# Kernel optimization log

Measured on AMD Instinct MI355X. Metric: run time of the kernel, lower is better.

Reference implementation:

```python
import jax, jax.numpy as jnp
import numpy as np
import math

D, H, F = 1024, 16, 4096
DH = D // H
EPS_LN = 1e-5


def _layernorm(x, scale, bias):
    mu = jnp.mean(x, axis=-1, keepdims=True)
    var = jnp.mean(jnp.square(x - mu), axis=-1, keepdims=True)
    return (x - mu) * jax.lax.rsqrt(var + EPS_LN) * scale + bias


def setup_inputs() -> dict:
    key = jax.random.key(0)
    ks = jax.random.split(key, 16)
    B, T = 2, 2048
    src = jax.random.normal(ks[0], (B, T, D), dtype=jnp.float32)
    attn_mask = jax.random.randint(ks[1], (T, T), 0, 2) == 1  # bool [T,S], True = masked
    xavier = lambda k, shp: jax.random.uniform(k, shp, jnp.float32, -1.0, 1.0) * math.sqrt(6.0 / (shp[0] + shp[1]))
    return {
        "src": src, "attn_mask": attn_mask,
        "q_w": xavier(ks[2], (D, D)), "q_b": jnp.zeros((D,), jnp.float32),
        "k_w": xavier(ks[3], (D, D)), "k_b": jnp.zeros((D,), jnp.float32),
        "v_w": xavier(ks[4], (D, D)), "v_b": jnp.zeros((D,), jnp.float32),
        "o_w": xavier(ks[5], (D, D)), "o_b": jnp.zeros((D,), jnp.float32),
        "l1_w": xavier(ks[6], (F, D)), "l1_b": jnp.zeros((F,), jnp.float32),
        "l2_w": xavier(ks[7], (D, F)), "l2_b": jnp.zeros((D,), jnp.float32),
        "n1_s": jnp.ones((D,), jnp.float32), "n1_b": jnp.zeros((D,), jnp.float32),
        "n2_s": jnp.ones((D,), jnp.float32), "n2_b": jnp.zeros((D,), jnp.float32),
        "alpha_attn": jax.random.normal(ks[8], (), jnp.float32) * 0.1,
        "alpha_ff": jax.random.normal(ks[9], (), jnp.float32) * 0.1,
    }


def reference(src, attn_mask, q_w, q_b, k_w, k_b, v_w, v_b, o_w, o_b,
              l1_w, l1_b, l2_w, l2_b, n1_s, n1_b, n2_s, n2_b,
              alpha_attn, alpha_ff):
    B, T, _ = src.shape
    # --- self-attention block (post-norm layer, dropout=0 => identity) ---
    q = (src @ q_w.T + q_b).reshape(B, T, H, DH).transpose(0, 2, 1, 3)  # [B,H,T,DH]
    k = (src @ k_w.T + k_b).reshape(B, T, H, DH).transpose(0, 2, 1, 3)
    v = (src @ v_w.T + v_b).reshape(B, T, H, DH).transpose(0, 2, 1, 3)
    scores = jnp.einsum('bhtd,bhsd->bhts', q, k) / math.sqrt(DH)  # [B,H,T,S]
    scores = jnp.where(attn_mask[None, None, :, :], -jnp.inf, scores)
    probs = jax.nn.softmax(scores + 1e-9, axis=-1)
    probs = jnp.where(jnp.isinf(scores), 0.0, probs)  # zero where masked (custom semantics)
    attn = jnp.einsum('bhts,bhsd->bhtd', probs, v).transpose(0, 2, 1, 3).reshape(B, T, D)
    attn = attn @ o_w.T + o_b
    x = _layernorm(src + alpha_attn * attn, n1_s, n1_b)
    # --- FFN block ---
    ff = jax.nn.relu(x @ l1_w.T + l1_b) @ l2_w.T + l2_b
    x = _layernorm(x + alpha_ff * ff, n2_s, n2_b)
    return x
```

## Files before the change

### kernel.cpp

```cpp
#include <hip/hip_runtime.h>
#include <math.h>

#define Dm 1024
#define Hh 16
#define DHd 64
#define Ff 4096
#define Tt 2048
#define Bb 2

#define ATT_C2 0.18033688011112042f

typedef __bf16 bf16_8 __attribute__((ext_vector_type(8)));
typedef __bf16 bf16x2 __attribute__((ext_vector_type(2)));
typedef __bf16 bf16x4 __attribute__((ext_vector_type(4)));
typedef float  f32x4  __attribute__((ext_vector_type(4)));

__device__ __forceinline__ unsigned short f2bf(float f) {
    unsigned int u = __float_as_uint(f);
    unsigned int r = (u + 0x7fffu + ((u >> 16) & 1u)) >> 16;
    return (unsigned short)r;
}

__device__ __forceinline__ bf16x2 pkbf(float a, float b) {
#if __has_builtin(__builtin_amdgcn_cvt_pk_bf16_f32)
    return __builtin_amdgcn_cvt_pk_bf16_f32(a, b);
#else
    bf16x2 r; r[0] = (__bf16)a; r[1] = (__bf16)b; return r;
#endif
}
__device__ __forceinline__ bf16x4 pkbf4(float a, float b, float c, float d) {
    bf16x2 lo = pkbf(a, b), hi = pkbf(c, d);
    return __builtin_shufflevector(lo, hi, 0, 1, 2, 3);
}

__device__ __forceinline__ void gld_lds16(const void* g, void* l) {
    __builtin_amdgcn_global_load_lds(
        (const __attribute__((address_space(1))) void*)g,
        (__attribute__((address_space(3))) void*)l,
        16, 0, 0);
}

__global__ __launch_bounds__(256) void preprocess_kernel(
    const float* __restrict__ q_w, const float* __restrict__ k_w,
    const float* __restrict__ v_w, const float* __restrict__ o_w,
    const float* __restrict__ l1_w, const float* __restrict__ l2_w,
    const float* __restrict__ src, const int* __restrict__ mask,
    const float* __restrict__ q_b, const float* __restrict__ k_b,
    unsigned short* __restrict__ qkw, unsigned short* __restrict__ vw16,
    unsigned short* __restrict__ ow,  unsigned short* __restrict__ l1w,
    unsigned short* __restrict__ l2w, unsigned short* __restrict__ srcb,
    unsigned* __restrict__ mbit, float* __restrict__ qkb)
{
    const int bid = blockIdx.x;
    const int tid = threadIdx.x;
    if (bid < 16384) {
        int i = bid * 256 + tid;
        const float* sp; unsigned short* dp; int off;
        if (i < 1048576) {
            if (i < 262144)      { sp = q_w; dp = qkw;           off = i; }
            else if (i < 524288) { sp = k_w; dp = qkw + 1048576; off = i - 262144; }
            else if (i < 786432) { sp = v_w; dp = vw16;          off = i - 524288; }
            else                 { sp = o_w; dp = ow;            off = i - 786432; }
        } else if (i < 2097152)  { sp = l1_w; dp = l1w;          off = i - 1048576; }
        else if (i < 3145728)    { sp = l2_w; dp = l2w;          off = i - 2097152; }
        else                     { sp = src;  dp = srcb;         off = i - 3145728; }
        float4 v = ((const float4*)sp)[off];
        ((bf16x4*)dp)[off] = pkbf4(v.x, v.y, v.z, v.w);
    } else if (bid < 16896) {
        int w = (bid - 16384) * 256 + tid;
        const int* p = mask + (size_t)w * 32;
        unsigned bits = 0;
        #pragma unroll
        for (int j = 0; j < 8; ++j) {
            int4 v = ((const int4*)p)[j];
            bits |= (v.x != 0 ? 1u : 0u) << (j * 4 + 0);
            bits |= (v.y != 0 ? 1u : 0u) << (j * 4 + 1);
            bits |= (v.z != 0 ? 1u : 0u) << (j * 4 + 2);
            bits |= (v.w != 0 ? 1u : 0u) << (j * 4 + 3);
        }
        mbit[w] = bits;
    } else {
        int i = (bid - 16896) * 256 + tid;
        qkb[i] = (i < 1024) ? q_b[i] : k_b[i - 1024];
    }
}

template<int RELU, int BF16OUT>
__global__ __launch_bounds__(256) void gemm_bf16_kernel(
    const unsigned short* __restrict__ A, const unsigned short* __restrict__ W,
    const float* __restrict__ bias, void* __restrict__ C, void* __restrict__ C2,
    int M, int N, int K, int ldc, int ksub)
{
    __shared__ __bf16 As[128][64];
    __shared__ __bf16 Bs[128][64];
    const int tid  = threadIdx.x;
    const int lane = tid & 63;
    const int wave = tid >> 6;
    const int m0 = blockIdx.y * 128;
    const int n0 = blockIdx.x * 128;
    const int lr8 = lane >> 3;
    const int gch = (lane & 7) ^ lr8;
    const int wm = (wave & 1) * 64;
    const int wn = (wave >> 1) * 64;
    const int quad = lane >> 4;
    const int lm = lane & 15;
    const int z  = blockIdx.z;
    const int kstart = z * ksub;
    void* Cz = (z == 0) ? C : C2;

    f32x4 acc[4][4];
    #pragma unroll
    for (int i = 0; i < 4; i++)
        #pragma unroll
        for (int j = 0; j < 4; j++) {
            acc[i][j][0] = 0.f; acc[i][j][1] = 0.f;
            acc[i][j][2] = 0.f; acc[i][j][3] = 0.f;
        }

    for (int k0 = kstart; k0 < kstart + ksub; k0 += 64) {
        __syncthreads();
        #pragma unroll
        for (int i = 0; i < 4; i++) {
            int seg = wave * 4 + i;
            int r = seg * 8 + lr8;
            gld_lds16(A + (size_t)(m0 + r) * K + k0 + gch * 8, &As[seg * 8][0]);
            gld_lds16(W + (size_t)(n0 + r) * K + k0 + gch * 8, &Bs[seg * 8][0]);
        }
        __syncthreads();
        #pragma unroll
        for (int kh = 0; kh < 2; kh++) {
            bf16_8 af[4], bfr[4];
            #pragma unroll
            for (int t = 0; t < 4; t++) {
                int ch = (kh * 4 + quad) ^ (lm & 7);
                af[t]  = *(const bf16_8*)&As[wm + t * 16 + lm][ch * 8];
                bfr[t] = *(const bf16_8*)&Bs[wn + t * 16 + lm][ch * 8];
            }
            #pragma unroll
            for (int i = 0; i < 4; i++)
                #pragma unroll
                for (int j = 0; j < 4; j++)
                    acc[i][j] = __builtin_amdgcn_mfma_f32_16x16x32_bf16(
                        af[i], bfr[j], acc[i][j], 0, 0, 0);
        }
    }

    float bvc[4];
    #pragma unroll
    for (int j = 0; j < 4; j++)
        bvc[j] = (z == 0) ? bias[n0 + wn + j * 16 + lm] : 0.f;

    #pragma unroll
    for (int i = 0; i < 4; i++)
        #pragma unroll
        for (int j = 0; j < 4; j++) {
            int col = n0 + wn + j * 16 + lm;
            #pragma unroll
            for (int r = 0; r < 4; r++) {
                int row = m0 + wm + i * 16 + quad * 4 + r;
                float v = acc[i][j][r] + bvc[j];
                if (RELU) v = fmaxf(v, 0.f);
                if (BF16OUT)
                    ((unsigned short*)Cz)[(size_t)row * ldc + col] = f2bf(v);
                else
                    ((float*)Cz)[(size_t)row * ldc + col] = v;
            }
        }
}

__global__ __launch_bounds__(256) void gemm_qkvt_kernel(
    const unsigned short* __restrict__ srcb, const unsigned short* __restrict__ qkw,
    const unsigned short* __restrict__ vw16, const float* __restrict__ qkb,
    const float* __restrict__ v_b,
    unsigned short* __restrict__ qk16, unsigned short* __restrict__ vtf)
{
    const int bid = blockIdx.x;
    const unsigned short *A, *W;
    const float* bias;
    unsigned short* C;
    int m0, n0, ldc;
    bool qscale, rowbias;
    if (bid < 512) {
        A = srcb; W = qkw; bias = qkb; C = qk16;
        n0 = (bid & 15) * 128; m0 = (bid >> 4) * 128;
        ldc = 2048; qscale = true; rowbias = false;
    } else {
        int b2 = bid - 512;
        A = vw16; W = srcb; bias = v_b; C = vtf;
        n0 = (b2 & 31) * 128; m0 = (b2 >> 5) * 128;
        ldc = 4096; qscale = false; rowbias = true;
    }
    const int K = 1024;

    __shared__ __bf16 As[128][64];
    __shared__ __bf16 Bs[128][64];
    const int tid  = threadIdx.x;
    const int lane = tid & 63;
    const int wave = tid >> 6;
    const int lr8 = lane >> 3;
    const int gch = (lane & 7) ^ lr8;
    const int wm = (wave & 1) * 64;
    const int wn = (wave >> 1) * 64;
    const int quad = lane >> 4;
    const int lm = lane & 15;

    f32x4 acc[4][4];
    #pragma unroll
    for (int i = 0; i < 4; i++)
        #pragma unroll
        for (int j = 0; j < 4; j++) {
            acc[i][j][0] = 0.f; acc[i][j][1] = 0.f;
            acc[i][j][2] = 0.f; acc[i][j][3] = 0.f;
        }

    for (int k0 = 0; k0 < K; k0 += 64) {
        __syncthreads();
        #pragma unroll
        for (int i = 0; i < 4; i++) {
            int seg = wave * 4 + i;
            int r = seg * 8 + lr8;
            gld_lds16(A + (size_t)(m0 + r) * K + k0 + gch * 8, &As[seg * 8][0]);
            gld_lds16(W + (size_t)(n0 + r) * K + k0 + gch * 8, &Bs[seg * 8][0]);
        }
        __syncthreads();
        #pragma unroll
        for (int kh = 0; kh < 2; kh++) {
            bf16_8 af[4], bfr[4];
            #pragma unroll
            for (int t = 0; t < 4; t++) {
                int ch = (kh * 4 + quad) ^ (lm & 7);
                af[t]  = *(const bf16_8*)&As[wm + t * 16 + lm][ch * 8];
                bfr[t] = *(const bf16_8*)&Bs[wn + t * 16 + lm][ch * 8];
            }
            #pragma unroll
            for (int i = 0; i < 4; i++)
                #pragma unroll
                for (int j = 0; j < 4; j++)
                    acc[i][j] = __builtin_amdgcn_mfma_f32_16x16x32_bf16(
                        af[i], bfr[j], acc[i][j], 0, 0, 0);
        }
    }

    float bvc[4];
    float brr[4][4];
    if (!rowbias) {
        #pragma unroll
        for (int j = 0; j < 4; j++) bvc[j] = bias[n0 + wn + j * 16 + lm];
    } else {
        #pragma unroll
        for (int i = 0; i < 4; i++) {
            float4 t4 = *(const float4*)&bias[m0 + wm + i * 16 + quad * 4];
            brr[i][0] = t4.x; brr[i][1] = t4.y; brr[i][2] = t4.z; brr[i][3] = t4.w;
        }
    }

    #pragma unroll
    for (int i = 0; i < 4; i++)
        #pragma unroll
        for (int j = 0; j < 4; j++) {
            int col = n0 + wn + j * 16 + lm;
            #pragma unroll
            for (int r = 0; r < 4; r++) {
                int row = m0 + wm + i * 16 + quad * 4 + r;
                float v = acc[i][j][r] + (rowbias ? brr[i][r] : bvc[j]);
                if (qscale && col < 1024) v *= ATT_C2;
                C[(size_t)row * ldc + col] = f2bf(v);
            }
        }
}

__global__ __launch_bounds__(256) void attn_mfma_kernel(
    const unsigned short* __restrict__ qk,
    const unsigned short* __restrict__ vt,
    const unsigned* __restrict__ mb,
    float* __restrict__ opart,
    float* __restrict__ lpart)
{
    __shared__ __bf16 Ks[128 * 64];
    __shared__ __bf16 Vt[64 * 128];
    __shared__ __bf16 Ps[4][32 * 64];

    const int tid  = threadIdx.x;
    const int lane = tid & 63;
    const int wave = tid >> 6;
    const int c    = lane & 15;
    const int quad = lane >> 4;
    const int bh = blockIdx.y;
    const int b = bh >> 4, h = bh & 15;
    const int t0 = blockIdx.x * 128;
    const int tw = t0 + wave * 32;
    const int z  = blockIdx.z;

    bf16_8 qf[2][2];
    #pragma unroll
    for (int tt = 0; tt < 2; ++tt)
        #pragma unroll
        for (int ks = 0; ks < 2; ++ks)
            qf[tt][ks] = *(const bf16_8*)(qk +
                (size_t)(b * Tt + tw + tt * 16 + c) * 2048 +
                h * DHd + quad * 8 + ks * 32);

    f32x4 oacc[2][4];
    f32x4 ol[2];
    #pragma unroll
    for (int tt = 0; tt < 2; ++tt) {
        ol[tt][0] = 0.f; ol[tt][1] = 0.f; ol[tt][2] = 0.f; ol[tt][3] = 0.f;
        #pragma unroll
        for (int dt = 0; dt < 4; ++dt) {
            oacc[tt][dt][0] = 0.f; oacc[tt][dt][1] = 0.f;
            oacc[tt][dt][2] = 0.f; oacc[tt][dt][3] = 0.f;
        }
    }
    bf16_8 vone;
    {
        __bf16 one = (__bf16)1.0f;
        #pragma unroll
        for (int j = 0; j < 8; ++j) vone[j] = one;
    }

    const int krow8 = lane >> 3;
    const int kj    = (lane & 7) ^ krow8;
    const int vr4   = lane >> 4;

    for (int st16 = z * 8; st16 < z * 8 + 8; ++st16) {
        const int s0 = st16 * 128;
        __syncthreads();

        #pragma unroll
        for (int i = 0; i < 4; ++i) {
            int ci = wave * 4 + i;
            {
                int r = 8 * ci + krow8;
                const unsigned short* g = qk +
                    (size_t)(b * Tt + s0 + r) * 2048 + 1024 + h * DHd + kj * 8;
                gld_lds16(g, &Ks[ci * 512]);
            }
            {
                int d = 4 * ci + vr4;
                int jj = (lane & 15) ^ (d & 7);
                const unsigned short* g = vt +
                    (size_t)(h * DHd + d) * 4096 + b * Tt + s0 + jj * 8;
                gld_lds16(g, &Vt[ci * 512]);
            }
        }

        unsigned mwv[2][4];
        #pragma unroll
        for (int tt = 0; tt < 2; ++tt)
            #pragma unroll
            for (int sp = 0; sp < 4; ++sp)
                mwv[tt][sp] = mb[(size_t)(tw + tt * 16 + c) * 64 + (s0 >> 5) + sp];

        __syncthreads();

        #pragma unroll
        for (int half = 0; half < 2; ++half) {
            #pragma unroll
            for (int s8l = 0; s8l < 4; ++s8l) {
                const int s8 = half * 4 + s8l;
                bf16_8 kf0 = *(const bf16_8*)&Ks[((s8 * 16 + c) * 8 + ((quad + 0) ^ (c & 7))) * 8];
                bf16_8 kf1 = *(const bf16_8*)&Ks[((s8 * 16 + c) * 8 + ((quad + 4) ^ (c & 7))) * 8];
                #pragma unroll
                for (int tt = 0; tt < 2; ++tt) {
                    f32x4 zr; zr[0] = 0.f; zr[1] = 0.f; zr[2] = 0.f; zr[3] = 0.f;
                    zr = __builtin_amdgcn_mfma_f32_16x16x32_bf16(kf0, qf[tt][0], zr, 0, 0, 0);
                    f32x4 sv = __builtin_amdgcn_mfma_f32_16x16x32_bf16(kf1, qf[tt][1], zr, 0, 0, 0);
                    unsigned mword = mwv[tt][s8 >> 1];
                    int bp = (s8 & 1) * 16 + quad * 4;
                    float p[4];
                    #pragma unroll
                    for (int r = 0; r < 4; ++r) {
                        int bit = (mword >> (bp + r)) & 1;
                        float x = bit ? -1e30f : sv[r];
                        p[r] = __builtin_amdgcn_exp2f(x);
                    }
                    bf16x4 pk4v = pkbf4(p[0], p[1], p[2], p[3]);
                    int trow = tt * 16 + c;
                    int ch = (s8l * 2 + (quad >> 1)) ^ (c & 7);
                    *(bf16x4*)&Ps[wave][trow * 64 + ch * 8 + (quad & 1) * 4] = pk4v;
                }
            }
            #pragma unroll
            for (int ks = 0; ks < 2; ++ks) {
                bf16_8 pa[2], vf[4];
                #pragma unroll
                for (int tt = 0; tt < 2; ++tt) {
                    int ch = (ks * 4 + quad) ^ (c & 7);
                    pa[tt] = *(const bf16_8*)&Ps[wave][(tt * 16 + c) * 64 + ch * 8];
                }
                #pragma unroll
                for (int dt = 0; dt < 4; ++dt) {
                    int sc = half * 8 + ks * 4 + quad;
                    int d = dt * 16 + c;
                    vf[dt] = *(const bf16_8*)&Vt[(d * 16 + (sc ^ (c & 7))) * 8];
                }
                #pragma unroll
                for (int tt = 0; tt < 2; ++tt) {
                    #pragma unroll
                    for (int dt = 0; dt < 4; ++dt)
                        oacc[tt][dt] = __builtin_amdgcn_mfma_f32_16x16x32_bf16(
                            pa[tt], vf[dt], oacc[tt][dt], 0, 0, 0);
                    ol[tt] = __builtin_amdgcn_mfma_f32_16x16x32_bf16(
                        pa[tt], vone, ol[tt], 0, 0, 0);
                }
            }
        }
    }

    float* op = opart + (size_t)z * 4194304;
    #pragma unroll
    for (int tt = 0; tt < 2; ++tt)
        #pragma unroll
        for (int r = 0; r < 4; ++r) {
            int row = b * Tt + tw + tt * 16 + quad * 4 + r;
            #pragma unroll
            for (int dt = 0; dt < 4; ++dt)
                op[(size_t)row * Dm + h * DHd + dt * 16 + c] = oacc[tt][dt][r];
            if (c == 0)
                lpart[z * 65536 + row * 16 + h] = ol[tt][r];
        }
}

__global__ __launch_bounds__(256) void combine_kernel(
    const float* __restrict__ opart, const float* __restrict__ lpart,
    unsigned short* __restrict__ atb)
{
    const int row = blockIdx.x;
    const int tid = threadIdx.x;
    const int h = tid >> 4;
    float l = lpart[row * 16 + h] + lpart[65536 + row * 16 + h];
    float inv = (l > 0.f) ? 1.f / l : 0.f;
    float4 a = ((const float4*)(opart + (size_t)row * Dm))[tid];
    float4 b = ((const float4*)(opart + 4194304 + (size_t)row * Dm))[tid];
    ((bf16x4*)(atb + (size_t)row * Dm))[tid] =
        pkbf4((a.x + b.x) * inv, (a.y + b.y) * inv,
              (a.z + b.z) * inv, (a.w + b.w) * inv);
}

template<int NPARTS, int BASEBF, int OUTF32, int OUTBF>
__global__ __launch_bounds__(256) void residual_ln_kernel(
    const void* __restrict__ base, const float* __restrict__ d0,
    const float* __restrict__ d1,
    const float* __restrict__ alpha_p, const float* __restrict__ scale,
    const float* __restrict__ bias, float* __restrict__ out,
    unsigned short* __restrict__ out_bf)
{
    const int row = blockIdx.x;
    const int tid = threadIdx.x;
    const float alpha = alpha_p[0];
    float4 xb;
    if (BASEBF) {
        bf16x4 bb = ((const bf16x4*)((const unsigned short*)base + (size_t)row * Dm))[tid];
        xb.x = (float)bb[0]; xb.y = (float)bb[1]; xb.z = (float)bb[2]; xb.w = (float)bb[3];
    } else {
        xb = ((const float4*)((const float*)base + (size_t)row * Dm))[tid];
    }
    float4 xd = ((const float4*)(d0 + (size_t)row * Dm))[tid];
    if (NPARTS == 2) {
        float4 x2 = ((const float4*)(d1 + (size_t)row * Dm))[tid];
        xd.x += x2.x; xd.y += x2.y; xd.z += x2.z; xd.w += x2.w;
    }
    float4 x;
    x.x = xb.x + alpha * xd.x;
    x.y = xb.y + alpha * xd.y;
    x.z = xb.z + alpha * xd.z;
    x.w = xb.w + alpha * xd.w;
    float s  = x.x + x.y + x.z + x.w;
    float sq = x.x*x.x + x.y*x.y + x.z*x.z + x.w*x.w;
    #pragma unroll
    for (int off = 32; off > 0; off >>= 1) {
        s  += __shfl_down(s, off, 64);
        sq += __shfl_down(sq, off, 64);
    }
    __shared__ float red[8];
    const int w = tid >> 6;
    if ((tid & 63) == 0) { red[w] = s; red[4 + w] = sq; }
    __syncthreads();
    s  = red[0] + red[1] + red[2] + red[3];
    sq = red[4] + red[5] + red[6] + red[7];
    const float mu  = s * (1.f / Dm);
    const float var = sq * (1.f / Dm) - mu * mu;
    const float r   = rsqrtf(var + 1e-5f);
    float4 sc = ((const float4*)scale)[tid];
    float4 bi = ((const float4*)bias)[tid];
    float4 o;
    o.x = (x.x - mu) * r * sc.x + bi.x;
    o.y = (x.y - mu) * r * sc.y + bi.y;
    o.z = (x.z - mu) * r * sc.z + bi.z;
    o.w = (x.w - mu) * r * sc.w + bi.w;
    if (OUTF32)
        ((float4*)(out + (size_t)row * Dm))[tid] = o;
    if (OUTBF)
        ((bf16x4*)(out_bf + (size_t)row * Dm))[tid] = pkbf4(o.x, o.y, o.z, o.w);
}

extern "C" void kernel_launch(void* const* d_in, const int* in_sizes, int n_in,
                              void* d_out, int out_size, void* d_ws, size_t ws_size,
                              hipStream_t stream)
{
    (void)in_sizes; (void)n_in; (void)out_size; (void)ws_size;
    const float* src  = (const float*)d_in[0];
    const int*   mask = (const int*)  d_in[1];
    const float* q_w  = (const float*)d_in[2];
    const float* q_b  = (const float*)d_in[3];
    const float* k_w  = (const float*)d_in[4];
    const float* k_b  = (const float*)d_in[5];
    const float* v_w  = (const float*)d_in[6];
    const float* v_b  = (const float*)d_in[7];
    const float* o_w  = (const float*)d_in[8];
    const float* o_b  = (const float*)d_in[9];
    const float* l1_w = (const float*)d_in[10];
    const float* l1_b = (const float*)d_in[11];
    const float* l2_w = (const float*)d_in[12];
    const float* l2_b = (const float*)d_in[13];
    const float* n1_s = (const float*)d_in[14];
    const float* n1_b = (const float*)d_in[15];
    const float* n2_s = (const float*)d_in[16];
    const float* n2_b = (const float*)d_in[17];
    const float* a_attn = (const float*)d_in[18];
    const float* a_ff   = (const float*)d_in[19];

    const size_t MB = 1024 * 1024;
    char* w = (char*)d_ws;
    unsigned short* qkw  = (unsigned short*)(w + 0);
    unsigned short* vw16 = (unsigned short*)(w + 4  * MB);
    unsigned short* ow   = (unsigned short*)(w + 6  * MB);
    unsigned short* l1w  = (unsigned short*)(w + 8  * MB);
    unsigned short* l2w  = (unsigned short*)(w + 16 * MB);
    unsigned short* srcb = (unsigned short*)(w + 24 * MB);
    unsigned short* qk16 = (unsigned short*)(w + 32 * MB);
    unsigned short* vtf  = (unsigned short*)(w + 48 * MB);
    unsigned*       mbit = (unsigned*)      (w + 56 * MB);
    float*          qkb  = (float*)         (w + 56 * MB + 524288);
    float*          lpart= (float*)         (w + 56 * MB + 655360);
    float*          opart= (float*)         (w + 58 * MB);
    unsigned short* atb  = (unsigned short*)(w + 24 * MB);
    float*          o0   = (float*)         (w + 58 * MB);
    float*          o1   = (float*)         (w + 74 * MB);
    unsigned short* x1b  = (unsigned short*)(w + 48 * MB);
    unsigned short* hb   = (unsigned short*)(w + 58 * MB);
    float*          fp0  = (float*)         (w + 0);
    float*          fp1  = (float*)         (w + 32 * MB);

    const int MR = Bb * Tt;
    dim3 blk(256);

    preprocess_kernel<<<dim3(16904), blk, 0, stream>>>(
        q_w, k_w, v_w, o_w, l1_w, l2_w, src, mask, q_b, k_b,
        qkw, vw16, ow, l1w, l2w, srcb, mbit, qkb);
    gemm_qkvt_kernel<<<dim3(768), blk, 0, stream>>>(
        srcb, qkw, vw16, qkb, v_b, qk16, vtf);
    attn_mfma_kernel<<<dim3(16, 32, 2), blk, 0, stream>>>(
        qk16, vtf, mbit, opart, lpart);
    combine_kernel<<<dim3(MR), blk, 0, stream>>>(opart, lpart, atb);
    gemm_bf16_kernel<0, 0><<<dim3(8, 32, 2), blk, 0, stream>>>(
        atb, ow, o_b, o0, o1, MR, Dm, Dm, Dm, 512);
    residual_ln_kernel<2, 0, 0, 1><<<dim3(MR), blk, 0, stream>>>(
        src, o0, o1, a_attn, n1_s, n1_b, nullptr, x1b);
    gemm_bf16_kernel<1, 1><<<dim3(32, 32, 1), blk, 0, stream>>>(
        x1b, l1w, l1_b, hb, nullptr, MR, Ff, Dm, Ff, Dm);
    gemm_bf16_kernel<0, 0><<<dim3(8, 32, 2), blk, 0, stream>>>(
        hb, l2w, l2_b, fp0, fp1, MR, Dm, Ff, Dm, Ff / 2);
    residual_ln_kernel<2, 1, 1, 0><<<dim3(MR), blk, 0, stream>>>(
        x1b, fp0, fp1, a_ff, n2_s, n2_b, (float*)d_out, nullptr);
}
```

Baseline: 398.1 us.

## Drop attention split-K combine and add a larger-tile FFN1 GEMM kernel

The attention kernel now walks the whole key range in one block and normalizes and writes bf16 output directly. This removes the split-K partial buffers and the separate combine kernel, at the cost of half the grid size for attention. A dedicated FFN1 GEMM uses 256x128 tiles with 4x8 MFMA accumulators per wave and a bias+ReLU epilogue, aiming for better operand reuse. The larger tile raises register pressure, and this GEMM has no double buffering.

```diff
diff --git a/kernel.cpp b/kernel.cpp
--- a/kernel.cpp
+++ b/kernel.cpp
@@ -168,6 +168,83 @@
         }
 }
 
+__global__ __launch_bounds__(256, 2) void gemm_ffn1_kernel(
+    const unsigned short* __restrict__ A, const unsigned short* __restrict__ W,
+    const float* __restrict__ bias, unsigned short* __restrict__ C)
+{
+    __shared__ __bf16 As[256][64];
+    __shared__ __bf16 Bs[128][64];
+    const int tid  = threadIdx.x;
+    const int lane = tid & 63;
+    const int wave = tid >> 6;
+    const int m0 = blockIdx.y * 256;
+    const int n0 = blockIdx.x * 128;
+    const int lr8 = lane >> 3;
+    const int gch = (lane & 7) ^ lr8;
+    const int quad = lane >> 4;
+    const int lm = lane & 15;
+
+    f32x4 acc[4][8];
+    #pragma unroll
+    for (int i = 0; i < 4; i++)
+        #pragma unroll
+        for (int j = 0; j < 8; j++) {
+            acc[i][j][0] = 0.f; acc[i][j][1] = 0.f;
+            acc[i][j][2] = 0.f; acc[i][j][3] = 0.f;
+        }
+
+    for (int k0 = 0; k0 < 1024; k0 += 64) {
+        __syncthreads();
+        #pragma unroll
+        for (int i = 0; i < 8; i++) {
+            int seg = wave * 8 + i;
+            int r = seg * 8 + lr8;
+            gld_lds16(A + (size_t)(m0 + r) * 1024 + k0 + gch * 8, &As[seg * 8][0]);
+        }
+        #pragma unroll
+        for (int i = 0; i < 4; i++) {
+            int seg = wave * 4 + i;
+            int r = seg * 8 + lr8;
+            gld_lds16(W + (size_t)(n0 + r) * 1024 + k0 + gch * 8, &Bs[seg * 8][0]);
+        }
+        __syncthreads();
+        #pragma unroll
+        for (int kh = 0; kh < 2; kh++) {
+            const int ch = (kh * 4 + quad) ^ (lm & 7);
+            bf16_8 af[4], bfr[8];
+            #pragma unroll
+            for (int t = 0; t < 4; t++)
+                af[t] = *(const bf16_8*)&As[wave * 64 + t * 16 + lm][ch * 8];
+            #pragma unroll
+            for (int j = 0; j < 8; j++)
+                bfr[j] = *(const bf16_8*)&Bs[j * 16 + lm][ch * 8];
+            #pragma unroll
+            for (int i = 0; i < 4; i++)
+                #pragma unroll
+                for (int j = 0; j < 8; j++)
+                    acc[i][j] = __builtin_amdgcn_mfma_f32_16x16x32_bf16(
+                        af[i], bfr[j], acc[i][j], 0, 0, 0);
+        }
+    }
+
+    float bv[8];
+    #pragma unroll
+    for (int j = 0; j < 8; j++) bv[j] = bias[n0 + j * 16 + lm];
+
+    #pragma unroll
+    for (int i = 0; i < 4; i++)
+        #pragma unroll
+        for (int j = 0; j < 8; j++) {
+            int col = n0 + j * 16 + lm;
+            #pragma unroll
+            for (int r = 0; r < 4; r++) {
+                int row = m0 + wave * 64 + i * 16 + quad * 4 + r;
+                float v = fmaxf(acc[i][j][r] + bv[j], 0.f);
+                C[(size_t)row * Ff + col] = f2bf(v);
+            }
+        }
+}
+
 __global__ __launch_bounds__(256) void gemm_qkvt_kernel(
     const unsigned short* __restrict__ srcb, const unsigned short* __restrict__ qkw,
     const unsigned short* __restrict__ vw16, const float* __restrict__ qkb,
@@ -273,8 +350,7 @@
     const unsigned short* __restrict__ qk,
     const unsigned short* __restrict__ vt,
     const unsigned* __restrict__ mb,
-    float* __restrict__ opart,
-    float* __restrict__ lpart)
+    unsigned short* __restrict__ out)
 {
     __shared__ __bf16 Ks[128 * 64];
     __shared__ __bf16 Vt[64 * 128];
@@ -289,7 +365,6 @@
     const int b = bh >> 4, h = bh & 15;
     const int t0 = blockIdx.x * 128;
     const int tw = t0 + wave * 32;
-    const int z  = blockIdx.z;
 
     bf16_8 qf[2][2];
     #pragma unroll
@@ -322,7 +397,7 @@
     const int kj    = (lane & 7) ^ krow8;
     const int vr4   = lane >> 4;
 
-    for (int st16 = z * 8; st16 < z * 8 + 8; ++st16) {
+    for (int st16 = 0; st16 < 16; ++st16) {
         const int s0 = st16 * 128;
         __syncthreads();
 
@@ -407,34 +482,18 @@
         }
     }
 
-    float* op = opart + (size_t)z * 4194304;
     #pragma unroll
     for (int tt = 0; tt < 2; ++tt)
         #pragma unroll
         for (int r = 0; r < 4; ++r) {
+            float l = ol[tt][r];
+            float inv = (l > 0.f) ? 1.f / l : 0.f;
             int row = b * Tt + tw + tt * 16 + quad * 4 + r;
             #pragma unroll
             for (int dt = 0; dt < 4; ++dt)
-                op[(size_t)row * Dm + h * DHd + dt * 16 + c] = oacc[tt][dt][r];
-            if (c == 0)
-                lpart[z * 65536 + row * 16 + h] = ol[tt][r];
-        }
-}
-
-__global__ __launch_bounds__(256) void combine_kernel(
-    const float* __restrict__ opart, const float* __restrict__ lpart,
-    unsigned short* __restrict__ atb)
-{
-    const int row = blockIdx.x;
-    const int tid = threadIdx.x;
-    const int h = tid >> 4;
-    float l = lpart[row * 16 + h] + lpart[65536 + row * 16 + h];
-    float inv = (l > 0.f) ? 1.f / l : 0.f;
-    float4 a = ((const float4*)(opart + (size_t)row * Dm))[tid];
-    float4 b = ((const float4*)(opart + 4194304 + (size_t)row * Dm))[tid];
-    ((bf16x4*)(atb + (size_t)row * Dm))[tid] =
-        pkbf4((a.x + b.x) * inv, (a.y + b.y) * inv,
-              (a.z + b.z) * inv, (a.w + b.w) * inv);
+                out[(size_t)row * Dm + h * DHd + dt * 16 + c] =
+                    f2bf(oacc[tt][dt][r] * inv);
+        }
 }
 
 template<int NPARTS, int BASEBF, int OUTF32, int OUTBF>
@@ -532,8 +591,6 @@
     unsigned short* vtf  = (unsigned short*)(w + 48 * MB);
     unsigned*       mbit = (unsigned*)      (w + 56 * MB);
     float*          qkb  = (float*)         (w + 56 * MB + 524288);
-    float*          lpart= (float*)         (w + 56 * MB + 655360);
-    float*          opart= (float*)         (w + 58 * MB);
     unsigned short* atb  = (unsigned short*)(w + 24 * MB);
     float*          o0   = (float*)         (w + 58 * MB);
     float*          o1   = (float*)         (w + 74 * MB);
@@ -550,15 +607,12 @@
         qkw, vw16, ow, l1w, l2w, srcb, mbit, qkb);
     gemm_qkvt_kernel<<<dim3(768), blk, 0, stream>>>(
         srcb, qkw, vw16, qkb, v_b, qk16, vtf);
-    attn_mfma_kernel<<<dim3(16, 32, 2), blk, 0, stream>>>(
-        qk16, vtf, mbit, opart, lpart);
-    combine_kernel<<<dim3(MR), blk, 0, stream>>>(opart, lpart, atb);
+    attn_mfma_kernel<<<dim3(16, 32), blk, 0, stream>>>(qk16, vtf, mbit, atb);
     gemm_bf16_kernel<0, 0><<<dim3(8, 32, 2), blk, 0, stream>>>(
         atb, ow, o_b, o0, o1, MR, Dm, Dm, Dm, 512);
     residual_ln_kernel<2, 0, 0, 1><<<dim3(MR), blk, 0, stream>>>(
         src, o0, o1, a_attn, n1_s, n1_b, nullptr, x1b);
-    gemm_bf16_kernel<1, 1><<<dim3(32, 32, 1), blk, 0, stream>>>(
-        x1b, l1w, l1_b, hb, nullptr, MR, Ff, Dm, Ff, Dm);
+    gemm_ffn1_kernel<<<dim3(32, 16), blk, 0, stream>>>(x1b, l1w, l1_b, hb);
     gemm_bf16_kernel<0, 0><<<dim3(8, 32, 2), blk, 0, stream>>>(
         hb, l2w, l2_b, fp0, fp1, MR, Dm, Ff, Dm, Ff / 2);
     residual_ln_kernel<2, 1, 1, 0><<<dim3(MR), blk, 0, stream>>>(
```

Result: faster. 369.7 us (-7.1%).
